# Kernel optimization log

Hardware: AMD Instinct MI355X
Metric: run time of the kernel (lower is better)

The kernel has to match this reference:

```python
import jax, jax.numpy as jnp
import numpy as np

D = 1024
H = 16

def setup_inputs() -> dict:
    key = jax.random.key(0)
    k1, k2, k3 = jax.random.split(key, 3)
    B, T = 4, 2048
    x = jax.random.normal(k1, (B, T, D), dtype=jnp.float32)
    # Linear weights stored as [in, out] so y = x @ W (equivalent to torch Linear with weight.T)
    W_attn = jax.random.normal(k2, (D, 3 * D), dtype=jnp.float32) * (1.0 / np.sqrt(D))
    W_proj = jax.random.normal(k3, (D, D), dtype=jnp.float32) * (1.0 / np.sqrt(D))
    return {"x": x, "W_attn": W_attn, "W_proj": W_proj}

def reference(x, W_attn, W_proj):
    B, T, _ = x.shape
    hd = D // H  # head dim
    qkv = x @ W_attn  # [B,T,3D]
    q, k, v = jnp.split(qkv, 3, axis=-1)
    # [B,T,D] -> [B,H,T,hd]
    q = q.reshape(B, T, H, hd).transpose(0, 2, 1, 3)
    k = k.reshape(B, T, H, hd).transpose(0, 2, 1, 3)
    v = v.reshape(B, T, H, hd).transpose(0, 2, 1, 3)
    scale = 1.0 / np.sqrt(hd).astype(np.float32)
    att = jnp.einsum('bhqd,bhkd->bhqk', q, k) * scale  # [B,H,T,T]
    causal = jnp.tril(jnp.ones((T, T), dtype=bool))
    att = jnp.where(causal[None, None], att, jnp.finfo(att.dtype).min)
    att = jax.nn.softmax(att, axis=-1)
    y = jnp.einsum('bhqk,bhkd->bhqd', att, v)  # [B,H,T,hd]
    y = y.transpose(0, 2, 1, 3).reshape(B, T, D)
    return y @ W_proj
```

## Files before the change

### kernel.cpp

```cpp
#include <hip/hip_runtime.h>


typedef __bf16 bf16;
typedef __attribute__((ext_vector_type(8))) __bf16 bf16x8;
typedef __attribute__((ext_vector_type(4))) __bf16 bf16x4;
typedef __attribute__((ext_vector_type(4))) float f4;

__device__ __forceinline__ void stage16(const bf16* g, bf16* l) {
    __builtin_amdgcn_global_load_lds((const __attribute__((address_space(1))) void*)g,
                                     (__attribute__((address_space(3))) void*)l,
                                     16, 0, 0);
}

__global__ __launch_bounds__(256)
void cast_f32_bf16(const float* __restrict__ src, bf16* __restrict__ dst, int n4)
{
    int i = blockIdx.x * 256 + threadIdx.x;
    if (i < n4) {
        float4 v = ((const float4*)src)[i];
        bf16x4 o = { (bf16)v.x, (bf16)v.y, (bf16)v.z, (bf16)v.w };
        *(bf16x4*)&dst[i * 4] = o;
    }
}

__global__ __launch_bounds__(256)
void transpose_f32_bf16(const float* __restrict__ src, bf16* __restrict__ dst,
                        int R, int C)
{
    __shared__ bf16 tile[64][65];
    int c0 = blockIdx.x * 64, r0 = blockIdx.y * 64;
    int tid = threadIdx.x;
    for (int i = tid; i < 64 * 64; i += 256) {
        int r = i >> 6, c = i & 63;
        tile[r][c] = (bf16)src[(long)(r0 + r) * C + c0 + c];
    }
    __syncthreads();
    for (int i = tid; i < 64 * 64; i += 256) {
        int r = i >> 6, c = i & 63;
        dst[(long)(c0 + r) * R + r0 + c] = tile[c][r];
    }
}

#define VMW6 asm volatile("s_waitcnt vmcnt(6)" ::: "memory")
#define VMW0 asm volatile("s_waitcnt vmcnt(0)" ::: "memory")
#define CLOB asm volatile("" ::: "memory")
#define BARR __builtin_amdgcn_s_barrier()
#define SB0  __builtin_amdgcn_sched_barrier(0)

template <typename OutT>
__global__ __launch_bounds__(512)
void gemm256(const bf16* __restrict__ A, const bf16* __restrict__ Bt,
             OutT* __restrict__ C, int lda, int ldb, int ldc, int K)
{
    extern __shared__ bf16 lds[];
    bf16* Asl = lds;
    bf16* Bsl = lds + 16384;
    int tid = threadIdx.x;
    int lane = tid & 63, wid = tid >> 6;
    int wm = wid >> 2, wn = wid & 3;
    int quad = lane >> 4, col = lane & 15;

    int nwg = gridDim.x * gridDim.y;
    int bid = blockIdx.y * gridDim.x + blockIdx.x;
    int swz = (bid & 7) * (nwg >> 3) + (bid >> 3);
    int bx = swz % gridDim.x, by = swz / gridDim.x;
    int m0 = by * 128, n0 = bx * 256;

    int NT = K >> 6;
    int srow = wid * 8 + (lane >> 3);
    int lincol = (lane & 7) * 8;
    int swcol  = ((lane & 7) ^ ((lane >> 3) & 7)) * 8;
    int xorv = (col & 7) << 4;
    int ke0 = ((quad * 16) ^ xorv) >> 1;
    int ke1 = ((quad * 16 + 64) ^ xorv) >> 1;

    f4 acc[4][4];
    #pragma unroll
    for (int mi = 0; mi < 4; ++mi)
        #pragma unroll
        for (int ni = 0; ni < 4; ++ni)
            acc[mi][ni] = (f4){0.f, 0.f, 0.f, 0.f};

    #define STG_HALF(mat, rb, ld, ts, dstb) do {                                \
        _Pragma("unroll")                                                       \
        for (int _i = 0; _i < 2; ++_i)                                          \
            stage16((mat) + (long)((rb) + _i * 64 + srow) * (ld) + (ts) * 64 + swcol, \
                    (dstb) + (_i * 64 + srow) * 64 + lincol);                   \
    } while (0)
    #define STGA(ts) STG_HALF(A, m0, lda, (ts), Asl + ((ts) & 1) * 8192)
    #define STGB(ts) do { bf16* _d = Bsl + ((ts) & 1) * 16384;                  \
        STG_HALF(Bt, n0,       ldb, (ts), _d);                                  \
        STG_HALF(Bt, n0 + 128, ldb, (ts), _d + 8192); } while (0)

    bf16x8 a[2][2], bb[4][2];
    #define RD_A(mp) do { _Pragma("unroll")                                     \
        for (int _m = 0; _m < 2; ++_m) {                                        \
            int _r = ab + ((mp) * 2 + _m) * 1024;                               \
            a[_m][0] = *(const bf16x8*)&Asl[_r + ke0];                          \
            a[_m][1] = *(const bf16x8*)&Asl[_r + ke1]; } } while (0)
    #define RD_B(np) do { _Pragma("unroll")                                     \
        for (int _n = 0; _n < 2; ++_n) {                                        \
            int _r = bbo + ((np) * 2 + _n) * 1024;                              \
            bb[(np)*2+_n][0] = *(const bf16x8*)&Bsl[_r + ke0];                  \
            bb[(np)*2+_n][1] = *(const bf16x8*)&Bsl[_r + ke1]; } } while (0)
    #define MM(mp, np) do { __builtin_amdgcn_s_setprio(1);                      \
        _Pragma("unroll")                                                       \
        for (int _m = 0; _m < 2; ++_m)                                          \
            _Pragma("unroll")                                                   \
            for (int _n = 0; _n < 2; ++_n)                                      \
                _Pragma("unroll")                                               \
                for (int kk = 0; kk < 2; ++kk)                                  \
                    acc[(mp)*2+_m][(np)*2+_n] =                                 \
                        __builtin_amdgcn_mfma_f32_16x16x32_bf16(                \
                            a[_m][kk], bb[(np)*2+_n][kk],                       \
                            acc[(mp)*2+_m][(np)*2+_n], 0, 0, 0);                \
        __builtin_amdgcn_s_setprio(0); } while (0)

    STGB(0); STGA(0); STGB(1); STGA(1);
    VMW6; CLOB; BARR; CLOB;

    for (int t = 0; t < NT; ++t) {
        int b = t & 1;
        int ab  = b * 8192  + (wm * 64 + col) * 64;
        int bbo = b * 16384 + (wn * 64 + col) * 64;
        RD_A(0); RD_B(0);
        CLOB; BARR; SB0; MM(0, 0); CLOB; BARR;
        RD_B(1);
        CLOB; BARR; SB0; MM(0, 1); CLOB; BARR;
        RD_A(1);
        if (t + 2 < NT) STGB(t + 2);
        CLOB; BARR; SB0; MM(1, 1); CLOB; BARR;
        if (t + 2 < NT) { STGA(t + 2); VMW6; }
        else if (t + 1 < NT) { VMW0; }
        CLOB; BARR; SB0; MM(1, 0); CLOB; BARR;
    }
    #undef STG_HALF
    #undef STGA
    #undef STGB
    #undef RD_A
    #undef RD_B
    #undef MM

    #pragma unroll
    for (int mi = 0; mi < 4; ++mi) {
        int rbase = m0 + wm * 64 + mi * 16 + quad * 4;
        #pragma unroll
        for (int ni = 0; ni < 4; ++ni) {
            int cc = n0 + wn * 64 + ni * 16 + col;
            #pragma unroll
            for (int r = 0; r < 4; ++r)
                C[(long)(rbase + r) * ldc + cc] = (OutT)acc[mi][ni][r];
        }
    }
}

#define QS 72
#define C_SL 0.18033688011112042f

__device__ __forceinline__ int vsw(int d, int k) {
    return d * 64 + ((((k >> 3) ^ (d & 7) ^ ((d >> 3) & 7)) & 7) << 3) + (k & 7);
}

__global__ __launch_bounds__(256)
void attn_mfma(bf16* __restrict__ qkv)
{
    __shared__ bf16 Ks[64 * QS];
    __shared__ bf16 Vt[64 * 64];
    __shared__ bf16 Ps[4 * 32 * QS];
    const int T = 2048, D3 = 3072;
    int tid = threadIdx.x;
    int lane = tid & 63, wid = tid >> 6;
    int quad = lane >> 4, col = lane & 15;
    int bh = blockIdx.x & 63;
    int qt = 15 - (blockIdx.x >> 6);
    int b = bh >> 4, h = bh & 15;
    long base = (long)b * T * D3 + h * 64;
    int q0 = qt * 128;
    int nk = 2 * qt + 2;
    int srow = tid >> 2, dseg = (tid & 3) * 16;
    bf16* Pw = &Ps[wid * 32 * QS];

    bf16x8 aq[2][2];
    #pragma unroll
    for (int nt = 0; nt < 2; ++nt) {
        const bf16* gq = &qkv[base + (long)(q0 + wid * 32 + nt * 16 + col) * D3 + quad * 8];
        aq[nt][0] = *(const bf16x8*)gq;
        aq[nt][1] = *(const bf16x8*)(gq + 32);
    }
    bf16 one1 = (bf16)1.0f;
    bf16x8 bones = {one1, one1, one1, one1, one1, one1, one1, one1};

    f4 of[2][4], lac[2];
    #pragma unroll
    for (int mg = 0; mg < 2; ++mg) {
        lac[mg] = (f4){0.f, 0.f, 0.f, 0.f};
        #pragma unroll
        for (int n = 0; n < 4; ++n) of[mg][n] = (f4){0.f, 0.f, 0.f, 0.f};
    }

    const bf16* g0 = &qkv[base + (long)srow * D3 + 1024 + dseg];
    bf16x8 kr0 = *(const bf16x8*)g0;
    bf16x8 kr1 = *(const bf16x8*)(g0 + 8);
    bf16x8 vr0 = *(const bf16x8*)(g0 + 1024);
    bf16x8 vr1 = *(const bf16x8*)(g0 + 1032);

    for (int kt = 0; kt < nk; ++kt) {
        __syncthreads();
        *(bf16x8*)&Ks[srow * QS + dseg]     = kr0;
        *(bf16x8*)&Ks[srow * QS + dseg + 8] = kr1;
        #pragma unroll
        for (int j = 0; j < 8; ++j) {
            Vt[vsw(dseg + j, srow)]     = vr0[j];
            Vt[vsw(dseg + 8 + j, srow)] = vr1[j];
        }
        if (kt + 1 < nk) {
            const bf16* gn = &qkv[base + (long)((kt + 1) * 64 + srow) * D3 + 1024 + dseg];
            kr0 = *(const bf16x8*)gn;
            kr1 = *(const bf16x8*)(gn + 8);
            vr0 = *(const bf16x8*)(gn + 1024);
            vr1 = *(const bf16x8*)(gn + 1032);
        }
        __syncthreads();
        bool diag = (kt >= nk - 2);
        int k0 = kt * 64;
        #pragma unroll
        for (int mt = 0; mt < 4; ++mt) {
            bf16x8 ak0 = *(const bf16x8*)&Ks[(mt * 16 + col) * QS + quad * 8];
            bf16x8 ak1 = *(const bf16x8*)&Ks[(mt * 16 + col) * QS + 32 + quad * 8];
            #pragma unroll
            for (int nt = 0; nt < 2; ++nt) {
                f4 z = (f4){0.f, 0.f, 0.f, 0.f};
                __builtin_amdgcn_s_setprio(1);
                z = __builtin_amdgcn_mfma_f32_16x16x32_bf16(ak0, aq[nt][0], z, 0, 0, 0);
                f4 st = __builtin_amdgcn_mfma_f32_16x16x32_bf16(ak1, aq[nt][1], z, 0, 0, 0);
                __builtin_amdgcn_s_setprio(0);
                bf16x4 pk;
                if (diag) {
                    int qg = q0 + wid * 32 + nt * 16 + col;
                    #pragma unroll
                    for (int r = 0; r < 4; ++r) {
                        float arg = fmaf(st[r], C_SL, -16.f);
                        if ((k0 + mt * 16 + quad * 4 + r) > qg) arg = -1e30f;
                        pk[r] = (bf16)exp2f(arg);
                    }
                } else {
                    #pragma unroll
                    for (int r = 0; r < 4; ++r)
                        pk[r] = (bf16)exp2f(fmaf(st[r], C_SL, -16.f));
                }
                *(bf16x4*)&Pw[(nt * 16 + col) * QS + mt * 16 + quad * 4] = pk;
            }
        }
        bf16x8 ap[2][2];
        #pragma unroll
        for (int mg = 0; mg < 2; ++mg) {
            ap[mg][0] = *(const bf16x8*)&Pw[(mg * 16 + col) * QS + quad * 8];
            ap[mg][1] = *(const bf16x8*)&Pw[(mg * 16 + col) * QS + 32 + quad * 8];
        }
        #pragma unroll
        for (int nd = 0; nd < 4; ++nd) {
            bf16x8 bv0 = *(const bf16x8*)&Vt[vsw(nd * 16 + col, quad * 8)];
            bf16x8 bv1 = *(const bf16x8*)&Vt[vsw(nd * 16 + col, 32 + quad * 8)];
            __builtin_amdgcn_s_setprio(1);
            of[0][nd] = __builtin_amdgcn_mfma_f32_16x16x32_bf16(ap[0][0], bv0, of[0][nd], 0, 0, 0);
            of[0][nd] = __builtin_amdgcn_mfma_f32_16x16x32_bf16(ap[0][1], bv1, of[0][nd], 0, 0, 0);
            of[1][nd] = __builtin_amdgcn_mfma_f32_16x16x32_bf16(ap[1][0], bv0, of[1][nd], 0, 0, 0);
            of[1][nd] = __builtin_amdgcn_mfma_f32_16x16x32_bf16(ap[1][1], bv1, of[1][nd], 0, 0, 0);
            __builtin_amdgcn_s_setprio(0);
        }
        __builtin_amdgcn_s_setprio(1);
        #pragma unroll
        for (int mg = 0; mg < 2; ++mg) {
            lac[mg] = __builtin_amdgcn_mfma_f32_16x16x32_bf16(ap[mg][0], bones, lac[mg], 0, 0, 0);
            lac[mg] = __builtin_amdgcn_mfma_f32_16x16x32_bf16(ap[mg][1], bones, lac[mg], 0, 0, 0);
        }
        __builtin_amdgcn_s_setprio(0);
    }
    #pragma unroll
    for (int mg = 0; mg < 2; ++mg)
        #pragma unroll
        for (int r = 0; r < 4; ++r) {
            float inv = 1.f / lac[mg][r];
            long yoff = base + (long)(q0 + wid * 32 + mg * 16 + quad * 4 + r) * D3;
            #pragma unroll
            for (int nd = 0; nd < 4; ++nd)
                qkv[yoff + nd * 16 + col] = (bf16)(of[mg][nd][r] * inv);
        }
}

extern "C" void kernel_launch(void* const* d_in, const int* in_sizes, int n_in,
                              void* d_out, int out_size, void* d_ws, size_t ws_size,
                              hipStream_t stream) {
    const float* x      = (const float*)d_in[0];
    const float* W_attn = (const float*)d_in[1];
    const float* W_proj = (const float*)d_in[2];
    float* out = (float*)d_out;

    bf16* qkv = (bf16*)d_ws;
    bf16* WtA = qkv + (size_t)8192 * 3072;
    bf16* WtP = WtA + (size_t)3072 * 1024;
    bf16* xb = (bf16*)d_out;

    static bool attr_set = false;
    if (!attr_set) {
        hipFuncSetAttribute((const void*)gemm256<bf16>,
                            hipFuncAttributeMaxDynamicSharedMemorySize, 98304);
        hipFuncSetAttribute((const void*)gemm256<float>,
                            hipFuncAttributeMaxDynamicSharedMemorySize, 98304);
        attr_set = true;
    }

    cast_f32_bf16<<<8192, 256, 0, stream>>>(x, xb, 8192 * 1024 / 4);
    transpose_f32_bf16<<<dim3(48, 16), 256, 0, stream>>>(W_attn, WtA, 1024, 3072);
    transpose_f32_bf16<<<dim3(16, 16), 256, 0, stream>>>(W_proj, WtP, 1024, 1024);
    gemm256<bf16><<<dim3(12, 64), 512, 98304, stream>>>(xb, WtA, qkv,
                                                        1024, 1024, 3072, 1024);
    attn_mfma<<<1024, 256, 0, stream>>>(qkv);
    gemm256<float><<<dim3(4, 64), 512, 98304, stream>>>(qkv, WtP, out,
                                                        3072, 1024, 1024, 1024);
}
```

Before: 255.6 us.

## Merge GEMM MFMA phases and vectorize V transpose into LDS with 4x4 blocks

In the GEMM main loop, the four barrier-separated MFMA phases are merged into two, cutting barrier count per k-step in half while keeping the global prefetch staging between them. In the attention kernel, each thread now loads a 4x4 block of V (four rows, four columns) and writes transposed 4-element vectors into the swizzled Vt LDS tile. This replaces sixteen scalar bf16 LDS stores per thread. Fewer barriers may reduce overlap of LDS reads with MFMA, and the V global loads become narrower 8-byte accesses across four rows.

Result: faster. 250.3 us (-2.1%).

```diff
diff --git a/kernel.cpp b/kernel.cpp
--- a/kernel.cpp
+++ b/kernel.cpp
@@ -123,16 +123,14 @@
         int b = t & 1;
         int ab  = b * 8192  + (wm * 64 + col) * 64;
         int bbo = b * 16384 + (wn * 64 + col) * 64;
-        RD_A(0); RD_B(0);
-        CLOB; BARR; SB0; MM(0, 0); CLOB; BARR;
-        RD_B(1);
-        CLOB; BARR; SB0; MM(0, 1); CLOB; BARR;
+        RD_A(0); RD_B(0); RD_B(1);
+        CLOB; BARR; SB0; MM(0, 0); MM(0, 1); CLOB; BARR;
         RD_A(1);
         if (t + 2 < NT) STGB(t + 2);
-        CLOB; BARR; SB0; MM(1, 1); CLOB; BARR;
+        CLOB; BARR; SB0; MM(1, 1); MM(1, 0);
         if (t + 2 < NT) { STGA(t + 2); VMW6; }
         else if (t + 1 < NT) { VMW0; }
-        CLOB; BARR; SB0; MM(1, 0); CLOB; BARR;
+        CLOB; BARR;
     }
     #undef STG_HALF
     #undef STGA
@@ -178,6 +176,7 @@
     int q0 = qt * 128;
     int nk = 2 * qt + 2;
     int srow = tid >> 2, dseg = (tid & 3) * 16;
+    int kg4 = (tid >> 4) * 4, dg4 = (tid & 15) * 4;
     bf16* Pw = &Ps[wid * 32 * QS];
 
     bf16x8 aq[2][2];
@@ -201,24 +200,27 @@
     const bf16* g0 = &qkv[base + (long)srow * D3 + 1024 + dseg];
     bf16x8 kr0 = *(const bf16x8*)g0;
     bf16x8 kr1 = *(const bf16x8*)(g0 + 8);
-    bf16x8 vr0 = *(const bf16x8*)(g0 + 1024);
-    bf16x8 vr1 = *(const bf16x8*)(g0 + 1032);
+    const bf16* gV = &qkv[base + (long)kg4 * D3 + 2048 + dg4];
+    bf16x4 vr[4];
+    #pragma unroll
+    for (int j = 0; j < 4; ++j) vr[j] = *(const bf16x4*)(gV + (long)j * D3);
 
     for (int kt = 0; kt < nk; ++kt) {
         __syncthreads();
         *(bf16x8*)&Ks[srow * QS + dseg]     = kr0;
         *(bf16x8*)&Ks[srow * QS + dseg + 8] = kr1;
         #pragma unroll
-        for (int j = 0; j < 8; ++j) {
-            Vt[vsw(dseg + j, srow)]     = vr0[j];
-            Vt[vsw(dseg + 8 + j, srow)] = vr1[j];
+        for (int i = 0; i < 4; ++i) {
+            bf16x4 c = { vr[0][i], vr[1][i], vr[2][i], vr[3][i] };
+            *(bf16x4*)&Vt[vsw(dg4 + i, kg4)] = c;
         }
         if (kt + 1 < nk) {
-            const bf16* gn = &qkv[base + (long)((kt + 1) * 64 + srow) * D3 + 1024 + dseg];
-            kr0 = *(const bf16x8*)gn;
-            kr1 = *(const bf16x8*)(gn + 8);
-            vr0 = *(const bf16x8*)(gn + 1024);
-            vr1 = *(const bf16x8*)(gn + 1032);
+            const bf16* gKn = &qkv[base + (long)((kt + 1) * 64 + srow) * D3 + 1024 + dseg];
+            kr0 = *(const bf16x8*)gKn;
+            kr1 = *(const bf16x8*)(gKn + 8);
+            const bf16* gVn = &qkv[base + (long)((kt + 1) * 64 + kg4) * D3 + 2048 + dg4];
+            #pragma unroll
+            for (int j = 0; j < 4; ++j) vr[j] = *(const bf16x4*)(gVn + (long)j * D3);
         }
         __syncthreads();
         bool diag = (kt >= nk - 2);
```
